# Performance work log

Measured on AMD Instinct MI355X. Metric: run time of the kernel, lower is better.

## Reference

```python
import jax, jax.numpy as jnp
import numpy as np

B, T, P, D, L = 16, 120, 96, 128, 2


def setup_inputs() -> dict:
    key = jax.random.key(0)
    k1, k2, k3, k4 = jax.random.split(key, 4)
    x = jax.random.normal(k1, (B, P, D, T), dtype=jnp.float32)
    # distances: symmetric-ish positive pairwise distances from random 3D points
    pts = jax.random.uniform(k2, (B, T, P, 3), dtype=jnp.float32) * 5.0
    diff = pts[:, :, :, None, :] - pts[:, :, None, :, :]
    distances = jnp.sqrt(jnp.sum(diff * diff, axis=-1) + 1e-12)
    # contiguous-prefix padding mask (matches the original self-loop loop semantics)
    counts = jax.random.randint(k3, (B,), P // 2, P + 1)
    padding_mask = jnp.arange(P)[None, :] < counts[:, None]
    # params: xavier_uniform with gain 1e-5 ~ tiny; bias 0; LN gamma=1, beta=0
    limit = 1e-5 * np.sqrt(6.0 / (D + D))
    W = jax.random.uniform(k4, (L, D, D), minval=-limit, maxval=limit, dtype=jnp.float32)
    b = jnp.zeros((L, D), dtype=jnp.float32)
    gamma = jnp.ones((L, D), dtype=jnp.float32)
    beta = jnp.zeros((L, D), dtype=jnp.float32)
    return {"x": x, "distances": distances, "padding_mask": padding_mask,
            "W": W, "b": b, "gamma": gamma, "beta": beta}


def _build_adjacency(distances, padding_mask):
    # valid_mask: [B,T,P,P]
    vm2d = (padding_mask[:, :, None] & padding_mask[:, None, :]).astype(distances.dtype)  # [B,P,P]
    vm = vm2d[:, None, :, :]
    vd = distances * vm
    pos = (vd > 0).astype(distances.dtype)
    n = jnp.sum(pos)
    mean = jnp.sum(vd * pos) / n
    var = jnp.sum(((vd - mean) ** 2) * pos) / (n - 1.0)  # unbiased, as torch.std
    sigma = jnp.sqrt(var) + 1e-8
    adj = jnp.exp(-(distances ** 2) / (2.0 * sigma ** 2)) * vm
    # self loops on valid (contiguous-prefix) nodes: add diag(mask)
    eye_mask = jnp.eye(P, dtype=distances.dtype)[None, :, :] * padding_mask[:, :, None].astype(distances.dtype)
    adj = adj + eye_mask[:, None, :, :]
    # symmetric normalization D^{-1/2} A D^{-1/2}
    deg = jnp.clip(jnp.sum(adj, axis=-1, keepdims=True), 1e-8, None)  # [B,T,P,1]
    deg = jnp.clip(deg * padding_mask[:, None, :, None].astype(distances.dtype), 1e-8, None)
    dis = deg ** -0.5
    adj = dis * adj * jnp.swapaxes(dis, -2, -1)
    return adj * vm


def _layer_norm_D(x, g, bt, eps=1e-5):
    # x: [B,P,D,T]; normalize over D axis
    mu = jnp.mean(x, axis=2, keepdims=True)
    var = jnp.mean((x - mu) ** 2, axis=2, keepdims=True)
    return (x - mu) * jax.lax.rsqrt(var + eps) * g[None, None, :, None] + bt[None, None, :, None]


def reference(x, distances, padding_mask, W, b, gamma, beta):
    adj = _build_adjacency(distances, padding_mask)  # [B,T,P,P]
    mask_f = padding_mask.astype(x.dtype)
    for l in range(L):
        xt = jnp.transpose(x, (0, 3, 1, 2))                      # [B,T,P,D]
        h = jnp.einsum('btpd,de->btpe', xt, W[l])                # x @ W
        o = jnp.einsum('btpq,btqd->btpd', adj, h)                # A @ xW
        o = jax.nn.relu(o + b[l])
        o = o * mask_f[:, None, :, None]
        o = jnp.transpose(o, (0, 2, 3, 1))                       # [B,P,D,T]
        o = _layer_norm_D(o, gamma[l], beta[l])
        x = x + o
    return x
```

## Files before the change

kernel.cpp:

```cpp
#include <hip/hip_runtime.h>
#include <math.h>

typedef __bf16 bf16_t;
typedef __bf16 bf16x8 __attribute__((ext_vector_type(8)));
typedef __bf16 bf16x4 __attribute__((ext_vector_type(4)));
typedef float f32x4 __attribute__((ext_vector_type(4)));

namespace {
constexpr int kB = 16;
constexpr int kT = 120;
constexpr int kP = 96;
constexpr int kD = 128;
constexpr int kBT = kB * kT;
constexpr int kPP = kP * kP;
constexpr int kPD = kP * kD;
constexpr long long kND = (long long)kBT * kPP;

constexpr int YS = 136;
constexpr int HS = 104;
constexpr int OS = 132;
constexpr int AS = 104;
constexpr int HT_OFF = 26112;
constexpr int AL_OFF = 52736;
constexpr int MROW_OFF = 72704;
constexpr int DIS_OFF = 73088;
constexpr int SMEM_B = 73472;
}

__device__ __forceinline__ f32x4 mfma16(bf16x8 a, bf16x8 b, f32x4 c) {
    return __builtin_amdgcn_mfma_f32_16x16x32_bf16(a, b, c, 0, 0, 0);
}

__global__ void k_prep(const float* __restrict__ W, bf16_t* __restrict__ wT,
                       const unsigned char* __restrict__ mraw, int* __restrict__ mask,
                       double* __restrict__ stats) {
    int bid = blockIdx.x;
    int l = bid >> 6;
    int idx = (bid & 63) * 256 + threadIdx.x;
    int n = idx >> 7, k = idx & 127;
    wT[l * 16384 + n * 128 + k] = (bf16_t)W[l * 16384 + k * 128 + n];

    if (bid == 0) {
        int tid = threadIdx.x;
        if (tid < 4) stats[tid] = 0.0;
        const unsigned int* u32 = (const unsigned int*)mraw;
        unsigned int w0 = u32[0];
        int mode;
        if (w0 == 0x01010101u) mode = 0;
        else if (w0 == 1u) mode = 1;
        else mode = 2;
        for (int i = tid; i < kB * kP; i += 256) {
            int v;
            if (mode == 0)      v = (mraw[i] != 0);
            else if (mode == 1) v = (u32[i] != 0);
            else                v = (((const float*)mraw)[i] != 0.0f);
            mask[i] = v;
        }
    }
}

__global__ __launch_bounds__(256) void k_stats(const float* __restrict__ dist,
                                               const int* __restrict__ mask,
                                               double* __restrict__ stats) {
    __shared__ int ml[kB * kP];
    for (int i = threadIdx.x; i < kB * kP; i += 256) ml[i] = mask[i];
    __syncthreads();

    long long n4 = kND / 4;
    long long stride = (long long)gridDim.x * 256;
    double s = 0.0, s2 = 0.0;
    int cnt = 0;
    for (long long i4 = (long long)blockIdx.x * 256 + threadIdx.x; i4 < n4; i4 += stride) {
        int q0 = 4 * (int)(i4 % 24);
        long long r = i4 / 24;
        int p = (int)(r % 96);
        int b = (int)((r / 96) / kT);
        const int* mb = ml + b * kP;
        if (mb[p]) {
            float4 d4 = *(const float4*)(dist + i4 * 4);
            if (mb[q0 + 0]) { s += d4.x; s2 += (double)d4.x * d4.x; cnt++; }
            if (mb[q0 + 1]) { s += d4.y; s2 += (double)d4.y * d4.y; cnt++; }
            if (mb[q0 + 2]) { s += d4.z; s2 += (double)d4.z * d4.z; cnt++; }
            if (mb[q0 + 3]) { s += d4.w; s2 += (double)d4.w * d4.w; cnt++; }
        }
    }
    __shared__ double sh[256];
    int tid = threadIdx.x;
    sh[tid] = s; __syncthreads();
    for (int off = 128; off > 0; off >>= 1) { if (tid < off) sh[tid] += sh[tid + off]; __syncthreads(); }
    if (tid == 0) atomicAdd(&stats[0], sh[0]);
    __syncthreads();
    sh[tid] = s2; __syncthreads();
    for (int off = 128; off > 0; off >>= 1) { if (tid < off) sh[tid] += sh[tid + off]; __syncthreads(); }
    if (tid == 0) atomicAdd(&stats[1], sh[0]);
    __syncthreads();
    sh[tid] = (double)cnt; __syncthreads();
    for (int off = 128; off > 0; off >>= 1) { if (tid < off) sh[tid] += sh[tid + off]; __syncthreads(); }
    if (tid == 0) atomicAdd(&stats[2], sh[0]);
}

__global__ __launch_bounds__(256) void k_tin(const float* __restrict__ x,
                                             bf16_t* __restrict__ y) {
    __shared__ float tile[64 * 121];
    int b = blockIdx.y, pd0 = blockIdx.x * 64;
    int tid = threadIdx.x;
    const float* xb = x + ((long long)b * kPD + pd0) * kT;
    #pragma unroll
    for (int k = 0; k < 8; ++k) {
        int idx = k * 256 + tid;
        if (idx < 1920) {
            int r = idx / 30, c = idx - r * 30;
            float4 v = *(const float4*)(xb + r * kT + c * 4);
            tile[r * 121 + c * 4 + 0] = v.x;
            tile[r * 121 + c * 4 + 1] = v.y;
            tile[r * 121 + c * 4 + 2] = v.z;
            tile[r * 121 + c * 4 + 3] = v.w;
        }
    }
    __syncthreads();
    bf16_t* yb = y + (long long)b * kT * kPD + pd0;
    #pragma unroll
    for (int k = 0; k < 4; ++k) {
        int idx = k * 256 + tid;
        if (idx < 960) {
            int t = idx >> 3, dg = idx & 7;
            bf16x8 o;
            #pragma unroll
            for (int j = 0; j < 8; ++j) o[j] = (bf16_t)tile[(dg * 8 + j) * 121 + t];
            *(bf16x8*)(yb + (long long)t * kPD + dg * 8) = o;
        }
    }
}

__global__ __launch_bounds__(256) void k_tout(const bf16_t* __restrict__ y,
                                              float* __restrict__ out) {
    __shared__ float tile[64 * 121];
    int b = blockIdx.y, pd0 = blockIdx.x * 64;
    int tid = threadIdx.x;
    const bf16_t* yb = y + (long long)b * kT * kPD + pd0;
    #pragma unroll
    for (int k = 0; k < 4; ++k) {
        int idx = k * 256 + tid;
        if (idx < 960) {
            int t = idx >> 3, dg = idx & 7;
            bf16x8 v = *(const bf16x8*)(yb + (long long)t * kPD + dg * 8);
            #pragma unroll
            for (int j = 0; j < 8; ++j) tile[(dg * 8 + j) * 121 + t] = (float)v[j];
        }
    }
    __syncthreads();
    float* ob = out + ((long long)b * kPD + pd0) * kT;
    #pragma unroll
    for (int k = 0; k < 8; ++k) {
        int idx = k * 256 + tid;
        if (idx < 1920) {
            int r = idx / 30, c = idx - r * 30;
            float4 v;
            v.x = tile[r * 121 + c * 4 + 0];
            v.y = tile[r * 121 + c * 4 + 1];
            v.z = tile[r * 121 + c * 4 + 2];
            v.w = tile[r * 121 + c * 4 + 3];
            *(float4*)(ob + r * kT + c * 4) = v;
        }
    }
}

__global__ __launch_bounds__(512, 2) void k_gcn(bf16_t* __restrict__ y,
                                                const float* __restrict__ dist,
                                                const int* __restrict__ mask,
                                                const double* __restrict__ stats,
                                                const bf16_t* __restrict__ wT,
                                                const float* __restrict__ bias,
                                                const float* __restrict__ gamma,
                                                const float* __restrict__ beta) {
    __shared__ __align__(16) char smem[SMEM_B];
    bf16_t* yL  = (bf16_t*)smem;
    bf16_t* hT  = (bf16_t*)(smem + HT_OFF);
    bf16_t* oLb = (bf16_t*)(smem + HT_OFF);
    float*  aT  = (float*)smem;
    bf16_t* aL  = (bf16_t*)(smem + AL_OFF);
    float* mrowf = (float*)(smem + MROW_OFF);
    float* dis   = (float*)(smem + DIS_OFF);

    const int tid = threadIdx.x;
    const int tx = tid & 15, ty = tid >> 4;
    const int lane = tid & 63, w = tid >> 6;
    const int wm = w >> 2, wn = w & 3;
    const int fc = lane & 15, fg = lane >> 4;
    const int bt = blockIdx.x, b = bt / kT;
    const int d0 = tx * 8;

    bf16_t* ybt = y + (size_t)bt * kPD;
    const float* dbt = dist + (size_t)bt * kPP;

    if (tid < kP) mrowf[tid] = (float)mask[b * kP + tid];

    double sn = stats[2];
    double mean = stats[0] / sn;
    double var = (stats[1] - sn * mean * mean) / (sn - 1.0);
    double sg = sqrt(var) + 1e-8;
    float inv2s2 = (float)(1.0 / (2.0 * sg * sg));

    __syncthreads();

    #pragma unroll
    for (int k = 0; k < 5; ++k) {
        int i4 = k * 512 + tid;
        if (i4 < 2304) {
            int e = i4 * 4;
            int p = e / kP, q = e - p * kP;
            float4 d4 = *(const float4*)(dbt + e);
            float mp = mrowf[p];
            float vv[4];
            vv[0] = (mp * mrowf[q + 0] != 0.f) ? __expf(-d4.x * d4.x * inv2s2) : 0.f;
            vv[1] = (mp * mrowf[q + 1] != 0.f) ? __expf(-d4.y * d4.y * inv2s2) : 0.f;
            vv[2] = (mp * mrowf[q + 2] != 0.f) ? __expf(-d4.z * d4.z * inv2s2) : 0.f;
            vv[3] = (mp * mrowf[q + 3] != 0.f) ? __expf(-d4.w * d4.w * inv2s2) : 0.f;
            #pragma unroll
            for (int j = 0; j < 4; ++j) {
                if (p == q + j) vv[j] += mp;
                aT[p * 100 + q + j] = vv[j];
            }
        }
    }
    __syncthreads();

    if (tid < kP) {
        float s = 0.f;
        for (int q = 0; q < kP; ++q) s += aT[q * 100 + tid];
        s = fmaxf(s, 1e-8f);
        s = fmaxf(s * mrowf[tid], 1e-8f);
        dis[tid] = rsqrtf(s);
    }
    __syncthreads();

    #pragma unroll
    for (int k = 0; k < 5; ++k) {
        int i4 = k * 512 + tid;
        if (i4 < 2304) {
            int e = i4 * 4;
            int p = e / kP, q = e - p * kP;
            float dp = dis[p];
            bf16x4 ov;
            #pragma unroll
            for (int j = 0; j < 4; ++j)
                ov[j] = (bf16_t)(dp * aT[p * 100 + q + j] * dis[q + j]);
            *(bf16x4*)(aL + p * AS + q) = ov;
        }
    }
    __syncthreads();

    #pragma unroll
    for (int i = 0; i < 3; ++i) {
        int p = ty * 3 + i;
        *(bf16x8*)(yL + p * YS + d0) = *(const bf16x8*)(ybt + p * kD + d0);
    }

    for (int l = 0; l < 2; ++l) {
        const bf16_t* wTl = wT + l * kD * kD;
        bf16x8 wf[4][2];
        #pragma unroll
        for (int kt = 0; kt < 4; ++kt) {
            wf[kt][0] = *(const bf16x8*)(wTl + ((wn * 2 + 0) * 16 + fc) * kD + kt * 32 + fg * 8);
            wf[kt][1] = *(const bf16x8*)(wTl + ((wn * 2 + 1) * 16 + fc) * kD + kt * 32 + fg * 8);
        }
        __syncthreads();

        f32x4 acc[3][2];
        #pragma unroll
        for (int mt = 0; mt < 3; ++mt) { acc[mt][0] = {0,0,0,0}; acc[mt][1] = {0,0,0,0}; }
        #pragma unroll
        for (int kt = 0; kt < 4; ++kt) {
            #pragma unroll
            for (int mt = 0; mt < 3; ++mt) {
                bf16x8 af = *(const bf16x8*)(yL + ((wm * 3 + mt) * 16 + fc) * YS + kt * 32 + fg * 8);
                acc[mt][0] = mfma16(af, wf[kt][0], acc[mt][0]);
                acc[mt][1] = mfma16(af, wf[kt][1], acc[mt][1]);
            }
        }
        #pragma unroll
        for (int mt = 0; mt < 3; ++mt)
            #pragma unroll
            for (int nn = 0; nn < 2; ++nn) {
                int e = (wn * 2 + nn) * 16 + fc;
                int p0 = (wm * 3 + mt) * 16 + fg * 4;
                bf16x4 hv = {(bf16_t)acc[mt][nn][0], (bf16_t)acc[mt][nn][1],
                             (bf16_t)acc[mt][nn][2], (bf16_t)acc[mt][nn][3]};
                *(bf16x4*)(hT + e * HS + p0) = hv;
            }
        __syncthreads();

        f32x4 acc2[3][2];
        #pragma unroll
        for (int mt = 0; mt < 3; ++mt) { acc2[mt][0] = {0,0,0,0}; acc2[mt][1] = {0,0,0,0}; }
        #pragma unroll
        for (int kt = 0; kt < 3; ++kt) {
            bf16x8 bf0 = *(const bf16x8*)(hT + ((wn * 2 + 0) * 16 + fc) * HS + kt * 32 + fg * 8);
            bf16x8 bf1 = *(const bf16x8*)(hT + ((wn * 2 + 1) * 16 + fc) * HS + kt * 32 + fg * 8);
            #pragma unroll
            for (int mt = 0; mt < 3; ++mt) {
                bf16x8 af = *(const bf16x8*)(aL + ((wm * 3 + mt) * 16 + fc) * AS + kt * 32 + fg * 8);
                acc2[mt][0] = mfma16(af, bf0, acc2[mt][0]);
                acc2[mt][1] = mfma16(af, bf1, acc2[mt][1]);
            }
        }
        __syncthreads();

        #pragma unroll
        for (int mt = 0; mt < 3; ++mt)
            #pragma unroll
            for (int nn = 0; nn < 2; ++nn) {
                int d = (wn * 2 + nn) * 16 + fc;
                int p0 = (wm * 3 + mt) * 16 + fg * 4;
                oLb[(p0 + 0) * OS + d] = (bf16_t)acc2[mt][nn][0];
                oLb[(p0 + 1) * OS + d] = (bf16_t)acc2[mt][nn][1];
                oLb[(p0 + 2) * OS + d] = (bf16_t)acc2[mt][nn][2];
                oLb[(p0 + 3) * OS + d] = (bf16_t)acc2[mt][nn][3];
            }
        __syncthreads();

        const float* bl = bias + l * kD;
        const float* gl = gamma + l * kD;
        const float* bel = beta + l * kD;
        float4 bb0 = *(const float4*)(bl + d0), bb1 = *(const float4*)(bl + d0 + 4);
        float4 gg0 = *(const float4*)(gl + d0), gg1 = *(const float4*)(gl + d0 + 4);
        float4 be0 = *(const float4*)(bel + d0), be1 = *(const float4*)(bel + d0 + 4);
        float bb[8] = {bb0.x, bb0.y, bb0.z, bb0.w, bb1.x, bb1.y, bb1.z, bb1.w};
        float gg[8] = {gg0.x, gg0.y, gg0.z, gg0.w, gg1.x, gg1.y, gg1.z, gg1.w};
        float be[8] = {be0.x, be0.y, be0.z, be0.w, be1.x, be1.y, be1.z, be1.w};

        #pragma unroll
        for (int i = 0; i < 3; ++i) {
            int p = ty * 3 + i;
            float mpf = mrowf[p];
            bf16x4 o0 = *(const bf16x4*)(oLb + p * OS + d0);
            bf16x4 o1 = *(const bf16x4*)(oLb + p * OS + d0 + 4);
            bf16x8 yv = *(const bf16x8*)(yL + p * YS + d0);
            float v[8];
            #pragma unroll
            for (int j = 0; j < 4; ++j) {
                v[j]     = fmaxf((float)o0[j] + bb[j], 0.f) * mpf;
                v[j + 4] = fmaxf((float)o1[j] + bb[j + 4], 0.f) * mpf;
            }
            float s = v[0] + v[1] + v[2] + v[3] + v[4] + v[5] + v[6] + v[7];
            s += __shfl_xor(s, 8);
            s += __shfl_xor(s, 4);
            s += __shfl_xor(s, 2);
            s += __shfl_xor(s, 1);
            float mu = s * 0.0078125f;

            float ss = 0.f;
            #pragma unroll
            for (int j = 0; j < 8; ++j) { float dv = v[j] - mu; ss += dv * dv; }
            ss += __shfl_xor(ss, 8);
            ss += __shfl_xor(ss, 4);
            ss += __shfl_xor(ss, 2);
            ss += __shfl_xor(ss, 1);
            float inv = rsqrtf(ss * 0.0078125f + 1e-5f);

            bf16x8 c;
            #pragma unroll
            for (int j = 0; j < 8; ++j)
                c[j] = (bf16_t)((float)yv[j] + (v[j] - mu) * inv * gg[j] + be[j]);

            if (l == 0) {
                *(bf16x8*)(yL + p * YS + d0) = c;
            } else {
                *(bf16x8*)(ybt + p * kD + d0) = c;
            }
        }
    }
}

extern "C" void kernel_launch(void* const* d_in, const int* in_sizes, int n_in,
                              void* d_out, int out_size, void* d_ws, size_t ws_size,
                              hipStream_t stream) {
    (void)in_sizes; (void)n_in; (void)out_size; (void)ws_size;

    const float* x = (const float*)d_in[0];
    const float* dist = (const float*)d_in[1];
    const unsigned char* mraw = (const unsigned char*)d_in[2];
    const float* W = (const float*)d_in[3];
    const float* bias = (const float*)d_in[4];
    const float* gamma = (const float*)d_in[5];
    const float* beta = (const float*)d_in[6];
    float* out = (float*)d_out;

    char* ws = (char*)d_ws;
    double* stats = (double*)ws;
    int* mask = (int*)(ws + 64);
    bf16_t* wT = (bf16_t*)(ws + 8192);
    bf16_t* y = (bf16_t*)(ws + 81920);

    k_prep<<<128, 256, 0, stream>>>(W, wT, mraw, mask, stats);
    k_stats<<<1024, 256, 0, stream>>>(dist, mask, stats);

    k_tin<<<dim3(kPD / 64, kB), 256, 0, stream>>>(x, y);

    k_gcn<<<kBT, 512, 0, stream>>>(y, dist, mask, stats, wT, bias, gamma, beta);

    k_tout<<<dim3(kPD / 64, kB), 256, 0, stream>>>(y, out);
}
```

Baseline: 183.9 us.

## Shrink GCN shared memory by keeping adjacency and residual in registers

Measured after the change: 203.7 us. 1.11x slower.

```diff
diff --git a/kernel.cpp b/kernel.cpp
--- a/kernel.cpp
+++ b/kernel.cpp
@@ -20,11 +20,11 @@
 constexpr int HS = 104;
 constexpr int OS = 132;
 constexpr int AS = 104;
-constexpr int HT_OFF = 26112;
-constexpr int AL_OFF = 52736;
-constexpr int MROW_OFF = 72704;
-constexpr int DIS_OFF = 73088;
-constexpr int SMEM_B = 73472;
+constexpr int AL_OFF = 26624;
+constexpr int MROW_OFF = 46592;
+constexpr int DIS_OFF = 46976;
+constexpr int DEG_OFF = 47360;
+constexpr int SMEM_B = 47744;
 }
 
 __device__ __forceinline__ f32x4 mfma16(bf16x8 a, bf16x8 b, f32x4 c) {
@@ -175,12 +175,12 @@
                                                 const float* __restrict__ beta) {
     __shared__ __align__(16) char smem[SMEM_B];
     bf16_t* yL  = (bf16_t*)smem;
-    bf16_t* hT  = (bf16_t*)(smem + HT_OFF);
-    bf16_t* oLb = (bf16_t*)(smem + HT_OFF);
-    float*  aT  = (float*)smem;
+    bf16_t* hT  = (bf16_t*)smem;
+    bf16_t* oLb = (bf16_t*)smem;
     bf16_t* aL  = (bf16_t*)(smem + AL_OFF);
     float* mrowf = (float*)(smem + MROW_OFF);
     float* dis   = (float*)(smem + DIS_OFF);
+    float* deg   = (float*)(smem + DEG_OFF);
 
     const int tid = threadIdx.x;
     const int tx = tid & 15, ty = tid >> 4;
@@ -193,7 +193,15 @@
     bf16_t* ybt = y + (size_t)bt * kPD;
     const float* dbt = dist + (size_t)bt * kPP;
 
-    if (tid < kP) mrowf[tid] = (float)mask[b * kP + tid];
+    bf16x8 yR[3];
+    #pragma unroll
+    for (int i = 0; i < 3; ++i)
+        yR[i] = *(const bf16x8*)(ybt + (ty * 3 + i) * kD + d0);
+
+    if (tid < kP) {
+        mrowf[tid] = (float)mask[b * kP + tid];
+        deg[tid] = 0.f;
+    }
 
     double sn = stats[2];
     double mean = stats[0] / sn;
@@ -203,6 +211,7 @@
 
     __syncthreads();
 
+    bf16x4 ev[5];
     #pragma unroll
     for (int k = 0; k < 5; ++k) {
         int i4 = k * 512 + tid;
@@ -219,16 +228,15 @@
             #pragma unroll
             for (int j = 0; j < 4; ++j) {
                 if (p == q + j) vv[j] += mp;
-                aT[p * 100 + q + j] = vv[j];
-            }
+                ev[k][j] = (bf16_t)vv[j];
+            }
+            atomicAdd(&deg[p], vv[0] + vv[1] + vv[2] + vv[3]);
         }
     }
     __syncthreads();
 
     if (tid < kP) {
-        float s = 0.f;
-        for (int q = 0; q < kP; ++q) s += aT[q * 100 + tid];
-        s = fmaxf(s, 1e-8f);
+        float s = fmaxf(deg[tid], 1e-8f);
         s = fmaxf(s * mrowf[tid], 1e-8f);
         dis[tid] = rsqrtf(s);
     }
@@ -244,17 +252,13 @@
             bf16x4 ov;
             #pragma unroll
             for (int j = 0; j < 4; ++j)
-                ov[j] = (bf16_t)(dp * aT[p * 100 + q + j] * dis[q + j]);
+                ov[j] = (bf16_t)(dp * (float)ev[k][j] * dis[q + j]);
             *(bf16x4*)(aL + p * AS + q) = ov;
         }
     }
-    __syncthreads();
-
-    #pragma unroll
-    for (int i = 0; i < 3; ++i) {
-        int p = ty * 3 + i;
-        *(bf16x8*)(yL + p * YS + d0) = *(const bf16x8*)(ybt + p * kD + d0);
-    }
+    #pragma unroll
+    for (int i = 0; i < 3; ++i)
+        *(bf16x8*)(yL + (ty * 3 + i) * YS + d0) = yR[i];
 
     for (int l = 0; l < 2; ++l) {
         const bf16_t* wTl = wT + l * kD * kD;
@@ -278,6 +282,8 @@
                 acc[mt][1] = mfma16(af, wf[kt][1], acc[mt][1]);
             }
         }
+        __syncthreads();
+
         #pragma unroll
         for (int mt = 0; mt < 3; ++mt)
             #pragma unroll
@@ -335,7 +341,6 @@
             float mpf = mrowf[p];
             bf16x4 o0 = *(const bf16x4*)(oLb + p * OS + d0);
             bf16x4 o1 = *(const bf16x4*)(oLb + p * OS + d0 + 4);
-            bf16x8 yv = *(const bf16x8*)(yL + p * YS + d0);
             float v[8];
             #pragma unroll
             for (int j = 0; j < 4; ++j) {
@@ -361,13 +366,19 @@
             bf16x8 c;
             #pragma unroll
             for (int j = 0; j < 8; ++j)
-                c[j] = (bf16_t)((float)yv[j] + (v[j] - mu) * inv * gg[j] + be[j]);
-
-            if (l == 0) {
-                *(bf16x8*)(yL + p * YS + d0) = c;
-            } else {
-                *(bf16x8*)(ybt + p * kD + d0) = c;
-            }
+                c[j] = (bf16_t)((float)yR[i][j] + (v[j] - mu) * inv * gg[j] + be[j]);
+            yR[i] = c;
+        }
+
+        if (l == 0) {
+            __syncthreads();
+            #pragma unroll
+            for (int i = 0; i < 3; ++i)
+                *(bf16x8*)(yL + (ty * 3 + i) * YS + d0) = yR[i];
+        } else {
+            #pragma unroll
+            for (int i = 0; i < 3; ++i)
+                *(bf16x8*)(ybt + (ty * 3 + i) * kD + d0) = yR[i];
         }
     }
 }
```
